# Performance work log

Hardware: AMD Instinct MI355X
Metric: run time of the kernel (lower is better)

Reference implementation:

```python
import jax, jax.numpy as jnp
from jax import lax
import numpy as np

DIM = 384
H = W = 32
B = 32
HALF = DIM // 2


def _parc(x, pe, w, b, axis):
    """Global circular depthwise conv along `axis` (2=H, 3=W). w: (C,1,kh,kw)."""
    x = x + pe
    k = x.shape[axis]
    if axis == 2:
        x_cat = jnp.concatenate([x, x[:, :, : k - 1, :]], axis=2)
    else:
        x_cat = jnp.concatenate([x, x[:, :, :, : k - 1]], axis=3)
    out = lax.conv_general_dilated(
        x_cat, w, window_strides=(1, 1), padding='VALID',
        dimension_numbers=('NCHW', 'OIHW', 'NCHW'),
        feature_group_count=x.shape[1])
    return out + b[None, :, None, None]


def setup_inputs() -> dict:
    key = jax.random.key(0)
    ks = jax.random.split(key, 12)
    std = 0.02
    return {
        'x': jax.random.normal(ks[0], (B, DIM, H, W), jnp.float32),
        'pe_h': std * jax.random.normal(ks[1], (1, HALF, H, 1), jnp.float32),
        'w_h': std * jax.random.normal(ks[2], (HALF, 1, H, 1), jnp.float32),
        'b_h': jnp.zeros((HALF,), jnp.float32),
        'pe_w': std * jax.random.normal(ks[3], (1, HALF, 1, W), jnp.float32),
        'w_w': std * jax.random.normal(ks[4], (HALF, 1, 1, W), jnp.float32),
        'b_w': jnp.zeros((HALF,), jnp.float32),
        'ln_w': jnp.ones((DIM,), jnp.float32),
        'ln_b': jnp.zeros((DIM,), jnp.float32),
        'w1': std * jax.random.normal(ks[5], (DIM, 4 * DIM), jnp.float32),
        'b1': jnp.zeros((4 * DIM,), jnp.float32),
        'w2': std * jax.random.normal(ks[6], (4 * DIM, DIM), jnp.float32),
        'b2': jnp.zeros((DIM,), jnp.float32),
        'gamma': 1e-6 * jnp.ones((DIM,), jnp.float32),
    }


def reference(x, pe_h, w_h, b_h, pe_w, w_w, b_w, ln_w, ln_b, w1, b1, w2, b2, gamma):
    inp = x
    half = x.shape[1] // 2
    x_h = _parc(x[:, :half], pe_h, w_h, b_h, axis=2)
    x_w = _parc(x[:, half:], pe_w, w_w, b_w, axis=3)
    y = jnp.concatenate([x_h, x_w], axis=1).transpose(0, 2, 3, 1)  # NHWC
    # LayerNorm over channels (eps=1e-6)
    mu = y.mean(-1, keepdims=True)
    var = ((y - mu) ** 2).mean(-1, keepdims=True)
    y = (y - mu) / jnp.sqrt(var + 1e-6) * ln_w + ln_b
    # inverted MLP: dim -> 4*dim -> dim with exact GELU
    y = jax.nn.gelu(jnp.dot(y, w1) + b1, approximate=False)
    y = jnp.dot(y, w2) + b2
    y = gamma * y
    return inp + y.transpose(0, 3, 1, 2)
```

## Files before the change

### kernel.cpp

```cpp
#include <hip/hip_runtime.h>


typedef __attribute__((ext_vector_type(8))) short short8;
typedef __attribute__((ext_vector_type(4))) float f32x4;
typedef __attribute__((ext_vector_type(16))) float f32x16;
typedef __attribute__((ext_vector_type(4))) int int4v;
typedef __attribute__((ext_vector_type(8))) int i32x8;

__device__ __forceinline__ float bf2f(unsigned short u) {
  union { unsigned int i; float f; } v; v.i = ((unsigned int)u) << 16; return v.f;
}
__device__ __forceinline__ unsigned short f2bf(float f) {
  union { float f; unsigned int i; } v; v.f = f;
  unsigned int r = v.i + 0x7FFFu + ((v.i >> 16) & 1u);
  return (unsigned short)(r >> 16);
}

#if defined(__has_builtin)
#if __has_builtin(__builtin_amdgcn_global_load_lds)
#define HAS_GLL 1
#endif
#endif
#ifndef HAS_GLL
#define HAS_GLL 0
#endif

#if HAS_GLL
__device__ __forceinline__ void gload16(const void* g, void* l) {
  __builtin_amdgcn_global_load_lds((const __attribute__((address_space(1))) void*)g,
                                   (__attribute__((address_space(3))) void*)l, 16, 0, 0);
}
#else
__device__ __forceinline__ void gload16(const void* g, void* l) {
  *(f32x4*)l = *(const f32x4*)g;
}
#endif

template <int N>
__device__ __forceinline__ void wait_vm() {
  asm volatile("s_waitcnt vmcnt(%0)" :: "n"(N) : "memory");
}
__device__ __forceinline__ void barrier_raw() {
  __builtin_amdgcn_s_barrier();
  __builtin_amdgcn_sched_barrier(0);
}

__device__ __forceinline__ float fast_gelu(float h) {
  const float e = __builtin_amdgcn_exp2f(-2.4554005f * h);
  return h * __builtin_amdgcn_rcpf(1.f + e);
}

__device__ __forceinline__ int pk4(float a, float b, float c, float d) {
  int r = __builtin_amdgcn_cvt_pk_fp8_f32(a, b, 0, false);
  return __builtin_amdgcn_cvt_pk_fp8_f32(c, d, r, true);
}

#define SCL1 0x7F7F7F7F

__device__ __forceinline__ int packed_off(int row, int kc) {
  return ((row >> 5) << 11) + ((kc & 1) << 10) + ((kc >> 1) << 9) + ((row & 31) << 4);
}

__global__ __launch_bounds__(256) void pack_kernel(
    const float* __restrict__ w1, const float* __restrict__ w2,
    char* __restrict__ w1p, char* __restrict__ w2p) {
  const int t = threadIdx.x;
  const int bid = blockIdx.x;
  float v[64];
  if (bid < 36) {
    const int kt = bid % 6, hg = bid / 6;
    const int h = hg * 256 + t;
    #pragma unroll
    for (int k = 0; k < 64; ++k) v[k] = w1[(size_t)(kt * 64 + k) * 1536 + h];
    char* base = w1p + (size_t)kt * 1536 * 64;
    #pragma unroll
    for (int k0 = 0; k0 < 64; k0 += 4) {
      *(int*)(base + packed_off(h, k0 >> 4) + (k0 & 12)) =
          pk4(v[k0], v[k0 + 1], v[k0 + 2], v[k0 + 3]);
    }
  } else {
    const int kt = bid - 36;
    for (int c = t; c < 384; c += 256) {
      #pragma unroll
      for (int k = 0; k < 64; ++k) v[k] = w2[(size_t)(kt * 64 + k) * 384 + c];
      char* base = w2p + (size_t)kt * 384 * 64;
      #pragma unroll
      for (int k0 = 0; k0 < 64; k0 += 4) {
        *(int*)(base + packed_off(c, k0 >> 4) + (k0 & 12)) =
            pk4(v[k0], v[k0 + 1], v[k0 + 2], v[k0 + 3]);
      }
    }
  }
}

__global__ __launch_bounds__(256) void conv_kernel(
    const float* __restrict__ x,
    const float* __restrict__ pe_h, const float* __restrict__ w_h, const float* __restrict__ b_h,
    const float* __restrict__ pe_w, const float* __restrict__ w_w, const float* __restrict__ b_w,
    unsigned short* __restrict__ convout) {
  __shared__ float wt_s[8][32], pe_s[8][32], pc_s[8][32];
  const int t = threadIdx.x;
  const int bid = blockIdx.x;
  const int b = bid / 48, g = bid % 48;
  const int c0 = g << 3;
  const bool ish = (c0 < 192);
  const int cl = t >> 5, q = t & 31;
  {
    const int c = c0 + cl;
    if (ish) { wt_s[cl][q] = w_h[(c << 5) + q];           pe_s[cl][q] = pe_h[(c << 5) + q]; }
    else     { const int cc = c - 192;
               wt_s[cl][q] = w_w[(cc << 5) + q];          pe_s[cl][q] = pe_w[(cc << 5) + q]; }
  }
  __syncthreads();
  {
    float s = ish ? b_h[c0 + cl] : b_w[c0 + cl - 192];
    #pragma unroll
    for (int i = 0; i < 32; ++i) s += pe_s[cl][(q + i) & 31] * wt_s[cl][i];
    pc_s[cl][q] = s;
  }
  __syncthreads();
  const float* xp = x + ((size_t)(b * 384 + c0 + cl) << 10);
  float col[32];
  if (ish) {
    #pragma unroll
    for (int j = 0; j < 32; ++j) col[j] = xp[(j << 5) + q];
  } else {
    const float* rp = xp + (q << 5);
    #pragma unroll
    for (int j4 = 0; j4 < 8; ++j4) {
      f32x4 v = *(const f32x4*)&rp[j4 << 2];
      col[j4 * 4 + 0] = v[0]; col[j4 * 4 + 1] = v[1];
      col[j4 * 4 + 2] = v[2]; col[j4 * 4 + 3] = v[3];
    }
  }
  float wr[32];
  #pragma unroll
  for (int i = 0; i < 32; ++i) wr[i] = wt_s[cl][i];
  float o[32];
  #pragma unroll
  for (int oo = 0; oo < 32; ++oo) o[oo] = pc_s[cl][oo];
  #pragma unroll
  for (int i = 0; i < 32; ++i)
    #pragma unroll
    for (int oo = 0; oo < 32; ++oo)
      o[oo] = fmaf(col[(oo + i) & 31], wr[i], o[oo]);
  unsigned short* op = convout + ((size_t)(b * 384 + c0 + cl) << 10);
  if (ish) {
    #pragma unroll
    for (int oo = 0; oo < 32; ++oo) op[(oo << 5) + q] = f2bf(o[oo]);
  } else {
    #pragma unroll
    for (int j8 = 0; j8 < 4; ++j8) {
      short8 p;
      #pragma unroll
      for (int j = 0; j < 8; ++j) p[j] = (short)f2bf(o[j8 * 8 + j]);
      *(short8*)&op[(q << 5) + j8 * 8] = p;
    }
  }
}

__global__ __launch_bounds__(256) void ln_stats_kernel(
    const unsigned short* __restrict__ conv,
    float* __restrict__ mu, float* __restrict__ rs) {
  __shared__ float sums[4][64], sqs[4][64];
  const int tid = threadIdx.x;
  const int lane = tid & 63;
  const int w = tid >> 6;
  const int px = blockIdx.x * 64 + lane;
  const int b = px >> 10, hw = px & 1023;
  const unsigned short* cp = conv + (((size_t)(b * 384 + w * 96)) << 10) + hw;
  float s = 0.f, ss = 0.f;
  #pragma unroll 8
  for (int k = 0; k < 96; ++k) {
    float v = bf2f(cp[(size_t)k << 10]);
    s += v; ss = fmaf(v, v, ss);
  }
  sums[w][lane] = s; sqs[w][lane] = ss;
  __syncthreads();
  if (tid < 64) {
    const float st = sums[0][tid] + sums[1][tid] + sums[2][tid] + sums[3][tid];
    const float sst = sqs[0][tid] + sqs[1][tid] + sqs[2][tid] + sqs[3][tid];
    const float m = st * (1.f / 384.f);
    const float var = sst * (1.f / 384.f) - m * m;
    mu[blockIdx.x * 64 + tid] = m;
    rs[blockIdx.x * 64 + tid] = rsqrtf(var + 1e-6f);
  }
}

__global__ __launch_bounds__(256) void ln_pack_kernel(
    const unsigned short* __restrict__ conv,
    const float* __restrict__ mu, const float* __restrict__ rs,
    char* __restrict__ ylnp,
    const float* __restrict__ ln_w, const float* __restrict__ ln_b) {
  __shared__ float lw[64], lb[64];
  const int kt = blockIdx.y;
  const int t = threadIdx.x;
  if (t < 64) { lw[t] = ln_w[kt * 64 + t]; lb[t] = ln_b[kt * 64 + t]; }
  __syncthreads();
  const int px = blockIdx.x * 256 + t;
  const int b = px >> 10, hw = px & 1023;
  const unsigned short* cp = conv + (((size_t)(b * 384 + kt * 64)) << 10) + hw;
  const float m = mu[px], r = rs[px];
  float ov[64];
  #pragma unroll
  for (int k = 0; k < 64; ++k) {
    const float v = bf2f(cp[(size_t)k << 10]);
    ov[k] = (v - m) * r * lw[k] + lb[k];
  }
  char* base = ylnp + (size_t)kt * 32768 * 64;
  #pragma unroll
  for (int q = 0; q < 4; ++q) {
    int4v d;
    d[0] = pk4(ov[q * 16 + 0],  ov[q * 16 + 1],  ov[q * 16 + 2],  ov[q * 16 + 3]);
    d[1] = pk4(ov[q * 16 + 4],  ov[q * 16 + 5],  ov[q * 16 + 6],  ov[q * 16 + 7]);
    d[2] = pk4(ov[q * 16 + 8],  ov[q * 16 + 9],  ov[q * 16 + 10], ov[q * 16 + 11]);
    d[3] = pk4(ov[q * 16 + 12], ov[q * 16 + 13], ov[q * 16 + 14], ov[q * 16 + 15]);
    *(int4v*)(base + packed_off(px, q)) = d;
  }
}

template <int EPI, int KDIM, int AROWS>
__global__ __launch_bounds__(512, 4) void gemm_kernel(
    const char* __restrict__ Ab, const char* __restrict__ Bb,
    char* __restrict__ Hout8, const float* __restrict__ bias,
    const float* __restrict__ gamma, const float* __restrict__ xres,
    float* __restrict__ out, int px0, int bstride, int boff, int hstride,
    int nwg, int nx) {
  extern __shared__ char lds[];
  constexpr int BM = 128, BN = 128;
  constexpr int NB = 3, DEPTH = 2;
  constexpr int NT = KDIM / 64;
  constexpr int SLOT = (BM + BN) * 64;
  constexpr int CH = 2;
  const int tid = threadIdx.x;
  const int lane = tid & 63;
  const int wid = tid >> 6;
  const int wm = wid >> 1;
  const int wn = wid & 1;
  const int lane31 = lane & 31;
  const int kh = lane >> 5;
  const int bid = blockIdx.x;
  const int q = nwg >> 3, r = nwg & 7;
  const int xcd = bid & 7, idx = bid >> 3;
  const int lg = (xcd < r ? xcd * (q + 1) : r * (q + 1) + (xcd - r) * q) + idx;
  const int xb = lg % nx, yb = lg / nx;
  const int arow0 = xb * BM;
  const int brow0 = yb * BN;

  f32x16 acc[2] = {};

  const int abase  = (wm << 11) + (kh << 9) + (lane31 << 4);
  const int bbase0 = BM * 64 + (((wn << 1) + 0) << 11) + (kh << 9) + (lane31 << 4);
  const int bbase1 = BM * 64 + (((wn << 1) + 1) << 11) + (kh << 9) + (lane31 << 4);

  auto stage = [&](int tile) {
    char* sl = lds + (tile % NB) * SLOT;
    gload16(Ab + ((size_t)tile * AROWS + arow0) * 64 + tid * 16, sl + tid * 16);
    gload16(Bb + ((size_t)tile * bstride + boff + brow0) * 64 + tid * 16,
            sl + BM * 64 + tid * 16);
  };

  auto step = [&](int t, int stage_tile) {
    const char* slp = lds + (t % NB) * SLOT;
    int4v a0  = *(const int4v*)(slp + abase);
    int4v a1  = *(const int4v*)(slp + abase + 1024);
    int4v b00 = *(const int4v*)(slp + bbase0);
    int4v b01 = *(const int4v*)(slp + bbase0 + 1024);
    int4v b10 = *(const int4v*)(slp + bbase1);
    int4v b11 = *(const int4v*)(slp + bbase1 + 1024);
    i32x8 av, bv0, bv1;
    av[0] = a0[0];  av[1] = a0[1];  av[2] = a0[2];  av[3] = a0[3];
    av[4] = a1[0];  av[5] = a1[1];  av[6] = a1[2];  av[7] = a1[3];
    bv0[0] = b00[0]; bv0[1] = b00[1]; bv0[2] = b00[2]; bv0[3] = b00[3];
    bv0[4] = b01[0]; bv0[5] = b01[1]; bv0[6] = b01[2]; bv0[7] = b01[3];
    bv1[0] = b10[0]; bv1[1] = b10[1]; bv1[2] = b10[2]; bv1[3] = b10[3];
    bv1[4] = b11[0]; bv1[5] = b11[1]; bv1[6] = b11[2]; bv1[7] = b11[3];
    if (stage_tile >= 0) stage(stage_tile);
    __builtin_amdgcn_s_setprio(1);
    acc[0] = __builtin_amdgcn_mfma_scale_f32_32x32x64_f8f6f4(
        av, bv0, acc[0], 0, 0, 0, SCL1, 0, SCL1);
    acc[1] = __builtin_amdgcn_mfma_scale_f32_32x32x64_f8f6f4(
        av, bv1, acc[1], 0, 0, 0, SCL1, 0, SCL1);
    __builtin_amdgcn_s_setprio(0);
  };

  #pragma unroll
  for (int d = 0; d < DEPTH; ++d) stage(d);
  wait_vm<CH * (DEPTH - 1)>();
  barrier_raw();

  #pragma unroll 1
  for (int t = 0; t < NT - DEPTH; ++t) {
    step(t, t + DEPTH);
    wait_vm<CH * (DEPTH - 1)>();
    barrier_raw();
  }
  step(NT - 2, -1);
  wait_vm<0>();
  barrier_raw();
  step(NT - 1, -1);

  if (EPI == 0) {
    const int kt2 = (arow0 >> 6) + (wm >> 1);
    #pragma unroll
    for (int G = 0; G < 4; ++G) {
      const int hbyte = ((wm & 1) << 5) + 8 * G + 4 * kh;
      const int hglob = arow0 + (wm << 5) + 8 * G + 4 * kh;
      const float c0 = bias[hglob + 0], c1 = bias[hglob + 1];
      const float c2 = bias[hglob + 2], c3 = bias[hglob + 3];
      const int kc = hbyte >> 4, sub = hbyte & 15;
      #pragma unroll
      for (int n = 0; n < 2; ++n) {
        const int px = brow0 + ((wn << 1) + n) * 32 + lane31;
        const int d = pk4(fast_gelu(acc[n][4 * G + 0] + c0),
                          fast_gelu(acc[n][4 * G + 1] + c1),
                          fast_gelu(acc[n][4 * G + 2] + c2),
                          fast_gelu(acc[n][4 * G + 3] + c3));
        *(int*)(Hout8 + (size_t)kt2 * hstride * 64 + packed_off(px, kc) + sub) = d;
      }
    }
  } else {
    #pragma unroll
    for (int G = 0; G < 4; ++G) {
      #pragma unroll
      for (int j = 0; j < 4; ++j) {
        const int c = arow0 + (wm << 5) + 8 * G + 4 * kh + j;
        const float gv = gamma[c];
        const float bvv = bias[c];
        #pragma unroll
        for (int n = 0; n < 2; ++n) {
          const int px = px0 + brow0 + ((wn << 1) + n) * 32 + lane31;
          const int bb = px >> 10, hw = px & 1023;
          const size_t oi = (((size_t)(bb * 384 + c)) << 10) + hw;
          out[oi] = xres[oi] + gv * (acc[n][4 * G + j] + bvv);
        }
      }
    }
  }
}

extern "C" void kernel_launch(void* const* d_in, const int* in_sizes, int n_in,
                              void* d_out, int out_size, void* d_ws, size_t ws_size,
                              hipStream_t stream) {
  (void)in_sizes; (void)n_in; (void)out_size;
  const float* x     = (const float*)d_in[0];
  const float* pe_h  = (const float*)d_in[1];
  const float* w_h   = (const float*)d_in[2];
  const float* b_h   = (const float*)d_in[3];
  const float* pe_w  = (const float*)d_in[4];
  const float* w_w   = (const float*)d_in[5];
  const float* b_w   = (const float*)d_in[6];
  const float* ln_w  = (const float*)d_in[7];
  const float* ln_b  = (const float*)d_in[8];
  const float* w1    = (const float*)d_in[9];
  const float* b1    = (const float*)d_in[10];
  const float* w2    = (const float*)d_in[11];
  const float* b2    = (const float*)d_in[12];
  const float* gamma = (const float*)d_in[13];
  float* out = (float*)d_out;
  char* ws = (char*)d_ws;

  char*           W1P  = ws;
  char*           W2P  = ws + 589824;
  float*          MU   = (float*)(ws + 1179648);
  float*          RS   = (float*)(ws + 1310720);
  char*           YLNP = ws + 1441792;
  unsigned short* CONV = (unsigned short*)(ws + 14024704);
  char*           HID  = ws + 14024704;

  int G = 32;
  while (G > 2) {
    size_t hid = (size_t)G * 1572864ull;
    size_t need = 14024704ull + (hid > 25165824ull ? hid : 25165824ull);
    if (need <= ws_size) break;
    G -= 2;
  }

  constexpr int LDS = (128 + 128) * 64 * 3;

  pack_kernel<<<dim3(60), dim3(256), 0, stream>>>(w1, w2, W1P, W2P);
  conv_kernel<<<dim3(1536), dim3(256), 0, stream>>>(x, pe_h, w_h, b_h, pe_w, w_w, b_w, CONV);
  ln_stats_kernel<<<dim3(512), dim3(256), 0, stream>>>(CONV, MU, RS);
  ln_pack_kernel<<<dim3(128, 6), dim3(256), 0, stream>>>(CONV, MU, RS, YLNP, ln_w, ln_b);
  for (int i0 = 0; i0 < 32; i0 += G) {
    const int gi = (32 - i0 < G) ? (32 - i0) : G;
    const int Mpx = gi * 1024;
    {
      const int nwg = 12 * (Mpx / 128);
      gemm_kernel<0, 384, 1536><<<dim3(nwg), dim3(512), LDS, stream>>>(
          W1P, YLNP, HID, b1, nullptr, nullptr, nullptr,
          0, 32768, i0 * 1024, Mpx, nwg, 12);
    }
    {
      const int nwg = 3 * (Mpx / 128);
      gemm_kernel<1, 1536, 384><<<dim3(nwg), dim3(512), LDS, stream>>>(
          W2P, HID, nullptr, b2, gamma, x, out, i0 * 1024, Mpx, 0, 0, nwg, 3);
    }
  }
}
```

Before: 110.6 us.

## Fuse LayerNorm stats and pack kernels; widen first GEMM tile to BN=256

Merges the two LayerNorm passes into one kernel that stages a 384x64 bf16 tile in LDS, computes mean and rstd, and writes the packed fp8 activations. The conv output is therefore read from global memory once instead of twice, and one launch goes away. The first GEMM also gets a BN template parameter set to 256, so each workgroup computes four 32-wide MFMA column fragments instead of two, halving the workgroup count and reusing each A tile more. The cost is more LDS per block (72 KB for the first GEMM and about 58 KB for the LN kernel) and more accumulator registers, which may lower occupancy.

After: 104.8 us. -5.2%, faster.

```diff
diff --git a/kernel.cpp b/kernel.cpp
--- a/kernel.cpp
+++ b/kernel.cpp
@@ -159,67 +159,67 @@
   }
 }
 
-__global__ __launch_bounds__(256) void ln_stats_kernel(
-    const unsigned short* __restrict__ conv,
-    float* __restrict__ mu, float* __restrict__ rs) {
-  __shared__ float sums[4][64], sqs[4][64];
-  const int tid = threadIdx.x;
-  const int lane = tid & 63;
-  const int w = tid >> 6;
-  const int px = blockIdx.x * 64 + lane;
-  const int b = px >> 10, hw = px & 1023;
-  const unsigned short* cp = conv + (((size_t)(b * 384 + w * 96)) << 10) + hw;
-  float s = 0.f, ss = 0.f;
-  #pragma unroll 8
-  for (int k = 0; k < 96; ++k) {
-    float v = bf2f(cp[(size_t)k << 10]);
-    s += v; ss = fmaf(v, v, ss);
-  }
-  sums[w][lane] = s; sqs[w][lane] = ss;
+__global__ __launch_bounds__(256) void ln_fused_kernel(
+    const unsigned short* __restrict__ conv, char* __restrict__ ylnp,
+    const float* __restrict__ ln_w, const float* __restrict__ ln_b) {
+  __shared__ unsigned short tile[384][72];
+  __shared__ float lws[384], lbs[384];
+  __shared__ float ps[4][64], pq[4][64];
+  __shared__ float mus[64], rss[64];
+  const int t = threadIdx.x;
+  const int pb = blockIdx.x;
+  const int b = pb >> 4;
+  const int hw0 = (pb & 15) << 6;
+  for (int i = t; i < 384; i += 256) { lws[i] = ln_w[i]; lbs[i] = ln_b[i]; }
+  #pragma unroll
+  for (int i = 0; i < 12; ++i) {
+    const int idx = t + i * 256;
+    const int c = idx >> 3, j = idx & 7;
+    short8 v = *(const short8*)(conv + (((size_t)(b * 384 + c)) << 10) + hw0 + j * 8);
+    *(short8*)&tile[c][j * 8] = v;
+  }
   __syncthreads();
-  if (tid < 64) {
-    const float st = sums[0][tid] + sums[1][tid] + sums[2][tid] + sums[3][tid];
-    const float sst = sqs[0][tid] + sqs[1][tid] + sqs[2][tid] + sqs[3][tid];
+  {
+    const int l = t & 63, qt = t >> 6;
+    float s = 0.f, ss = 0.f;
+    #pragma unroll
+    for (int k = 0; k < 96; ++k) {
+      const float v = bf2f(tile[qt * 96 + k][l]);
+      s += v; ss = fmaf(v, v, ss);
+    }
+    ps[qt][l] = s; pq[qt][l] = ss;
+  }
+  __syncthreads();
+  if (t < 64) {
+    const float st = ps[0][t] + ps[1][t] + ps[2][t] + ps[3][t];
+    const float sq = pq[0][t] + pq[1][t] + pq[2][t] + pq[3][t];
     const float m = st * (1.f / 384.f);
-    const float var = sst * (1.f / 384.f) - m * m;
-    mu[blockIdx.x * 64 + tid] = m;
-    rs[blockIdx.x * 64 + tid] = rsqrtf(var + 1e-6f);
-  }
-}
-
-__global__ __launch_bounds__(256) void ln_pack_kernel(
-    const unsigned short* __restrict__ conv,
-    const float* __restrict__ mu, const float* __restrict__ rs,
-    char* __restrict__ ylnp,
-    const float* __restrict__ ln_w, const float* __restrict__ ln_b) {
-  __shared__ float lw[64], lb[64];
-  const int kt = blockIdx.y;
-  const int t = threadIdx.x;
-  if (t < 64) { lw[t] = ln_w[kt * 64 + t]; lb[t] = ln_b[kt * 64 + t]; }
+    const float var = sq * (1.f / 384.f) - m * m;
+    mus[t] = m; rss[t] = rsqrtf(var + 1e-6f);
+  }
   __syncthreads();
-  const int px = blockIdx.x * 256 + t;
-  const int b = px >> 10, hw = px & 1023;
-  const unsigned short* cp = conv + (((size_t)(b * 384 + kt * 64)) << 10) + hw;
-  const float m = mu[px], r = rs[px];
-  float ov[64];
-  #pragma unroll
-  for (int k = 0; k < 64; ++k) {
-    const float v = bf2f(cp[(size_t)k << 10]);
-    ov[k] = (v - m) * r * lw[k] + lb[k];
-  }
-  char* base = ylnp + (size_t)kt * 32768 * 64;
-  #pragma unroll
-  for (int q = 0; q < 4; ++q) {
+  const int l = t & 63, kc = t >> 6;
+  const int px = pb * 64 + l;
+  const float m = mus[l], r = rss[l];
+  #pragma unroll
+  for (int kt = 0; kt < 6; ++kt) {
+    const int c0 = kt * 64 + kc * 16;
+    float ov[16];
+    #pragma unroll
+    for (int e = 0; e < 16; ++e) {
+      const float v = bf2f(tile[c0 + e][l]);
+      ov[e] = (v - m) * r * lws[c0 + e] + lbs[c0 + e];
+    }
     int4v d;
-    d[0] = pk4(ov[q * 16 + 0],  ov[q * 16 + 1],  ov[q * 16 + 2],  ov[q * 16 + 3]);
-    d[1] = pk4(ov[q * 16 + 4],  ov[q * 16 + 5],  ov[q * 16 + 6],  ov[q * 16 + 7]);
-    d[2] = pk4(ov[q * 16 + 8],  ov[q * 16 + 9],  ov[q * 16 + 10], ov[q * 16 + 11]);
-    d[3] = pk4(ov[q * 16 + 12], ov[q * 16 + 13], ov[q * 16 + 14], ov[q * 16 + 15]);
-    *(int4v*)(base + packed_off(px, q)) = d;
-  }
-}
-
-template <int EPI, int KDIM, int AROWS>
+    d[0] = pk4(ov[0],  ov[1],  ov[2],  ov[3]);
+    d[1] = pk4(ov[4],  ov[5],  ov[6],  ov[7]);
+    d[2] = pk4(ov[8],  ov[9],  ov[10], ov[11]);
+    d[3] = pk4(ov[12], ov[13], ov[14], ov[15]);
+    *(int4v*)(ylnp + (size_t)kt * 32768 * 64 + packed_off(px, kc)) = d;
+  }
+}
+
+template <int EPI, int KDIM, int AROWS, int BN>
 __global__ __launch_bounds__(512, 4) void gemm_kernel(
     const char* __restrict__ Ab, const char* __restrict__ Bb,
     char* __restrict__ Hout8, const float* __restrict__ bias,
@@ -227,11 +227,13 @@
     float* __restrict__ out, int px0, int bstride, int boff, int hstride,
     int nwg, int nx) {
   extern __shared__ char lds[];
-  constexpr int BM = 128, BN = 128;
+  constexpr int BM = 128;
+  constexpr int FN = BN / 64;
   constexpr int NB = 3, DEPTH = 2;
   constexpr int NT = KDIM / 64;
   constexpr int SLOT = (BM + BN) * 64;
-  constexpr int CH = 2;
+  constexpr int CH = (BM + BN) * 4 / 512;
+  constexpr int BCH = BN * 4 / 512;
   const int tid = threadIdx.x;
   const int lane = tid & 63;
   const int wid = tid >> 6;
@@ -247,40 +249,44 @@
   const int arow0 = xb * BM;
   const int brow0 = yb * BN;
 
-  f32x16 acc[2] = {};
-
-  const int abase  = (wm << 11) + (kh << 9) + (lane31 << 4);
-  const int bbase0 = BM * 64 + (((wn << 1) + 0) << 11) + (kh << 9) + (lane31 << 4);
-  const int bbase1 = BM * 64 + (((wn << 1) + 1) << 11) + (kh << 9) + (lane31 << 4);
+  f32x16 acc[FN] = {};
+
+  const int abase = (wm << 11) + (kh << 9) + (lane31 << 4);
+  int bbase[FN];
+  #pragma unroll
+  for (int n = 0; n < FN; ++n)
+    bbase[n] = BM * 64 + ((wn * FN + n) << 11) + (kh << 9) + (lane31 << 4);
 
   auto stage = [&](int tile) {
     char* sl = lds + (tile % NB) * SLOT;
     gload16(Ab + ((size_t)tile * AROWS + arow0) * 64 + tid * 16, sl + tid * 16);
-    gload16(Bb + ((size_t)tile * bstride + boff + brow0) * 64 + tid * 16,
-            sl + BM * 64 + tid * 16);
+    const char* bsrc = Bb + ((size_t)tile * bstride + boff + brow0) * 64;
+    #pragma unroll
+    for (int i = 0; i < BCH; ++i)
+      gload16(bsrc + (i * 512 + tid) * 16, sl + BM * 64 + (i * 512 + tid) * 16);
   };
 
   auto step = [&](int t, int stage_tile) {
     const char* slp = lds + (t % NB) * SLOT;
-    int4v a0  = *(const int4v*)(slp + abase);
-    int4v a1  = *(const int4v*)(slp + abase + 1024);
-    int4v b00 = *(const int4v*)(slp + bbase0);
-    int4v b01 = *(const int4v*)(slp + bbase0 + 1024);
-    int4v b10 = *(const int4v*)(slp + bbase1);
-    int4v b11 = *(const int4v*)(slp + bbase1 + 1024);
-    i32x8 av, bv0, bv1;
-    av[0] = a0[0];  av[1] = a0[1];  av[2] = a0[2];  av[3] = a0[3];
-    av[4] = a1[0];  av[5] = a1[1];  av[6] = a1[2];  av[7] = a1[3];
-    bv0[0] = b00[0]; bv0[1] = b00[1]; bv0[2] = b00[2]; bv0[3] = b00[3];
-    bv0[4] = b01[0]; bv0[5] = b01[1]; bv0[6] = b01[2]; bv0[7] = b01[3];
-    bv1[0] = b10[0]; bv1[1] = b10[1]; bv1[2] = b10[2]; bv1[3] = b10[3];
-    bv1[4] = b11[0]; bv1[5] = b11[1]; bv1[6] = b11[2]; bv1[7] = b11[3];
+    int4v a0 = *(const int4v*)(slp + abase);
+    int4v a1 = *(const int4v*)(slp + abase + 1024);
+    i32x8 av;
+    av[0] = a0[0]; av[1] = a0[1]; av[2] = a0[2]; av[3] = a0[3];
+    av[4] = a1[0]; av[5] = a1[1]; av[6] = a1[2]; av[7] = a1[3];
+    i32x8 bv[FN];
+    #pragma unroll
+    for (int n = 0; n < FN; ++n) {
+      int4v p0 = *(const int4v*)(slp + bbase[n]);
+      int4v p1 = *(const int4v*)(slp + bbase[n] + 1024);
+      bv[n][0] = p0[0]; bv[n][1] = p0[1]; bv[n][2] = p0[2]; bv[n][3] = p0[3];
+      bv[n][4] = p1[0]; bv[n][5] = p1[1]; bv[n][6] = p1[2]; bv[n][7] = p1[3];
+    }
     if (stage_tile >= 0) stage(stage_tile);
     __builtin_amdgcn_s_setprio(1);
-    acc[0] = __builtin_amdgcn_mfma_scale_f32_32x32x64_f8f6f4(
-        av, bv0, acc[0], 0, 0, 0, SCL1, 0, SCL1);
-    acc[1] = __builtin_amdgcn_mfma_scale_f32_32x32x64_f8f6f4(
-        av, bv1, acc[1], 0, 0, 0, SCL1, 0, SCL1);
+    #pragma unroll
+    for (int n = 0; n < FN; ++n)
+      acc[n] = __builtin_amdgcn_mfma_scale_f32_32x32x64_f8f6f4(
+          av, bv[n], acc[n], 0, 0, 0, SCL1, 0, SCL1);
     __builtin_amdgcn_s_setprio(0);
   };
 
@@ -310,8 +316,8 @@
       const float c2 = bias[hglob + 2], c3 = bias[hglob + 3];
       const int kc = hbyte >> 4, sub = hbyte & 15;
       #pragma unroll
-      for (int n = 0; n < 2; ++n) {
-        const int px = brow0 + ((wn << 1) + n) * 32 + lane31;
+      for (int n = 0; n < FN; ++n) {
+        const int px = brow0 + (wn * FN + n) * 32 + lane31;
         const int d = pk4(fast_gelu(acc[n][4 * G + 0] + c0),
                           fast_gelu(acc[n][4 * G + 1] + c1),
                           fast_gelu(acc[n][4 * G + 2] + c2),
@@ -328,8 +334,8 @@
         const float gv = gamma[c];
         const float bvv = bias[c];
         #pragma unroll
-        for (int n = 0; n < 2; ++n) {
-          const int px = px0 + brow0 + ((wn << 1) + n) * 32 + lane31;
+        for (int n = 0; n < FN; ++n) {
+          const int px = px0 + brow0 + (wn * FN + n) * 32 + lane31;
           const int bb = px >> 10, hw = px & 1023;
           const size_t oi = (((size_t)(bb * 384 + c)) << 10) + hw;
           out[oi] = xres[oi] + gv * (acc[n][4 * G + j] + bvv);
@@ -362,8 +368,6 @@
 
   char*           W1P  = ws;
   char*           W2P  = ws + 589824;
-  float*          MU   = (float*)(ws + 1179648);
-  float*          RS   = (float*)(ws + 1310720);
   char*           YLNP = ws + 1441792;
   unsigned short* CONV = (unsigned short*)(ws + 14024704);
   char*           HID  = ws + 14024704;
@@ -376,24 +380,26 @@
     G -= 2;
   }
 
-  constexpr int LDS = (128 + 128) * 64 * 3;
+  constexpr int LDS1 = (128 + 256) * 64 * 3;
+  constexpr int LDS2 = (128 + 128) * 64 * 3;
+  (void)hipFuncSetAttribute((const void*)gemm_kernel<0, 384, 1536, 256>,
+                            hipFuncAttributeMaxDynamicSharedMemorySize, LDS1);
 
   pack_kernel<<<dim3(60), dim3(256), 0, stream>>>(w1, w2, W1P, W2P);
   conv_kernel<<<dim3(1536), dim3(256), 0, stream>>>(x, pe_h, w_h, b_h, pe_w, w_w, b_w, CONV);
-  ln_stats_kernel<<<dim3(512), dim3(256), 0, stream>>>(CONV, MU, RS);
-  ln_pack_kernel<<<dim3(128, 6), dim3(256), 0, stream>>>(CONV, MU, RS, YLNP, ln_w, ln_b);
+  ln_fused_kernel<<<dim3(512), dim3(256), 0, stream>>>(CONV, YLNP, ln_w, ln_b);
   for (int i0 = 0; i0 < 32; i0 += G) {
     const int gi = (32 - i0 < G) ? (32 - i0) : G;
     const int Mpx = gi * 1024;
     {
-      const int nwg = 12 * (Mpx / 128);
-      gemm_kernel<0, 384, 1536><<<dim3(nwg), dim3(512), LDS, stream>>>(
+      const int nwg = 12 * (Mpx / 256);
+      gemm_kernel<0, 384, 1536, 256><<<dim3(nwg), dim3(512), LDS1, stream>>>(
           W1P, YLNP, HID, b1, nullptr, nullptr, nullptr,
           0, 32768, i0 * 1024, Mpx, nwg, 12);
     }
     {
       const int nwg = 3 * (Mpx / 128);
-      gemm_kernel<1, 1536, 384><<<dim3(nwg), dim3(512), LDS, stream>>>(
+      gemm_kernel<1, 1536, 384, 128><<<dim3(nwg), dim3(512), LDS2, stream>>>(
           W2P, HID, nullptr, b2, gamma, x, out, i0 * 1024, Mpx, 0, 0, nwg, 3);
     }
   }
```
